# Kernel optimization log

Measured on AMD Instinct MI355X. Metric: run time of the kernel, lower is better.

Reference implementation:

```python
import jax, jax.numpy as jnp
import numpy as np

N_NODES = 50000
N_EDGES = 800000
D_FEAT = 64


def setup_inputs() -> dict:
    key = jax.random.key(0)
    k1, k2, k3, k4 = jax.random.split(key, 4)
    row_idx = jnp.sort(jax.random.randint(k1, (N_EDGES,), 0, N_NODES, dtype=jnp.int32))
    col_idx = jax.random.randint(k2, (N_EDGES,), 0, N_NODES, dtype=jnp.int32)
    vals = jax.random.uniform(k3, (N_EDGES,), dtype=jnp.float32)
    embeds = jax.random.normal(k4, (N_NODES, D_FEAT), dtype=jnp.float32)
    return {"row_idx": row_idx, "col_idx": col_idx, "vals": vals, "embeds": embeds}


def reference(row_idx, col_idx, vals, embeds):
    # SpMM: out[r] = sum_{e: row[e]==r} vals[e] * embeds[col[e]]
    gathered = vals[:, None] * embeds[col_idx]          # [E, D]
    out = jax.ops.segment_sum(gathered, row_idx, num_segments=N_NODES)  # [N, D]
    return out
```

## Files before the change

### kernel.cpp

```cpp
#include <hip/hip_runtime.h>


constexpr int N_NODES = 50000;
constexpr int N_EDGES = 800000;
constexpr int D_FEAT  = 64;

__global__ __launch_bounds__(256) void build_row_ptr_kernel(
    const int* __restrict__ row_idx,
    int*       __restrict__ row_ptr)
{
    const int e = blockIdx.x * blockDim.x + threadIdx.x;
    if (e >= N_EDGES) return;
    const int r     = row_idx[e];
    const int rprev = (e == 0) ? -1 : row_idx[e - 1];
    for (int q = rprev + 1; q <= r; ++q) row_ptr[q] = e;
    if (e == N_EDGES - 1) {
        for (int q = r + 1; q <= N_NODES; ++q) row_ptr[q] = N_EDGES;
    }
}

__global__ __launch_bounds__(256) void gcn_spmm_rows_kernel(
    const int*   __restrict__ row_ptr,
    const int*   __restrict__ col_idx,
    const float* __restrict__ vals,
    const float* __restrict__ embeds,
    float*       __restrict__ out)
{
    const int gtid = blockIdx.x * blockDim.x + threadIdx.x;
    const int row  = gtid >> 6;
    if (row >= N_NODES) return;
    const int lane = threadIdx.x & 63;
    const int q    = lane >> 4;
    const int f    = lane & 15;

    const int s = row_ptr[row];
    const int e = row_ptr[row + 1];

    const float4* __restrict__ emb4 = (const float4*)embeds;

    float4 a0 = make_float4(0.f, 0.f, 0.f, 0.f);
    float4 a1 = make_float4(0.f, 0.f, 0.f, 0.f);

    int base = s + q;
    for (; base + 4 < e; base += 8) {
        const int   c0 = col_idx[base];
        const float v0 = vals[base];
        const int   c1 = col_idx[base + 4];
        const float v1 = vals[base + 4];
        const float4 g0 = emb4[c0 * 16 + f];
        const float4 g1 = emb4[c1 * 16 + f];
        a0.x += v0 * g0.x; a0.y += v0 * g0.y; a0.z += v0 * g0.z; a0.w += v0 * g0.w;
        a1.x += v1 * g1.x; a1.y += v1 * g1.y; a1.z += v1 * g1.z; a1.w += v1 * g1.w;
    }
    if (base < e) {
        const int   c0 = col_idx[base];
        const float v0 = vals[base];
        const float4 g0 = emb4[c0 * 16 + f];
        a0.x += v0 * g0.x; a0.y += v0 * g0.y; a0.z += v0 * g0.z; a0.w += v0 * g0.w;
    }

    float x = a0.x + a1.x;
    float y = a0.y + a1.y;
    float z = a0.z + a1.z;
    float w = a0.w + a1.w;

    x += __shfl_xor(x, 16); x += __shfl_xor(x, 32);
    y += __shfl_xor(y, 16); y += __shfl_xor(y, 32);
    z += __shfl_xor(z, 16); z += __shfl_xor(z, 32);
    w += __shfl_xor(w, 16); w += __shfl_xor(w, 32);

    if (q == 0) {
        ((float4*)out)[row * 16 + f] = make_float4(x, y, z, w);
    }
}

extern "C" void kernel_launch(void* const* d_in, const int* in_sizes, int n_in,
                              void* d_out, int out_size, void* d_ws, size_t ws_size,
                              hipStream_t stream) {
    const int*   row_idx = (const int*)  d_in[0];
    const int*   col_idx = (const int*)  d_in[1];
    const float* vals    = (const float*)d_in[2];
    const float* embeds  = (const float*)d_in[3];
    float*       out     = (float*)      d_out;
    int*         row_ptr = (int*)        d_ws;

    {
        const int block  = 256;
        const int blocks = (N_EDGES + block - 1) / block;
        build_row_ptr_kernel<<<blocks, block, 0, stream>>>(row_idx, row_ptr);
    }
    {
        const int block  = 256;
        const int blocks = (N_NODES * 64 + block - 1) / block;
        gcn_spmm_rows_kernel<<<blocks, block, 0, stream>>>(row_ptr, col_idx, vals,
                                                           embeds, out);
    }
}
```

Baseline: 101.3 us.

## Split feature dimension into slices across blocks, one edge per lane group

Each wavefront now handles one row and only a 16-float slice of the features. Its 16 lane groups each take a different edge, and 4 lanes per group load a float4 each. Eight consecutive blocks cover two row-quads across four slices. This is meant to raise memory-level parallelism on rows averaging 16 edges, but each col_idx/vals element is now read four times, the grid is four times larger, and the final reduction needs more shuffle steps.

After: 129.0 us. 1.27x slower.

```diff
diff --git a/kernel.cpp b/kernel.cpp
--- a/kernel.cpp
+++ b/kernel.cpp
@@ -19,58 +19,54 @@
     }
 }
 
-__global__ __launch_bounds__(256) void gcn_spmm_rows_kernel(
+__global__ __launch_bounds__(256) void gcn_spmm_sliced_kernel(
     const int*   __restrict__ row_ptr,
     const int*   __restrict__ col_idx,
     const float* __restrict__ vals,
     const float* __restrict__ embeds,
     float*       __restrict__ out)
 {
-    const int gtid = blockIdx.x * blockDim.x + threadIdx.x;
-    const int row  = gtid >> 6;
+    const int b = blockIdx.x;
+    const int x = b & 7;
+    const int s = x & 3;
+    const int i = ((b >> 3) << 1) + (x >> 2);
+    const int row = (i << 2) + (threadIdx.x >> 6);
     if (row >= N_NODES) return;
+
     const int lane = threadIdx.x & 63;
-    const int q    = lane >> 4;
-    const int f    = lane & 15;
+    const int g    = lane >> 2;
+    const int h    = lane & 3;
 
-    const int s = row_ptr[row];
-    const int e = row_ptr[row + 1];
+    const int s_ = row_ptr[row];
+    const int e_ = row_ptr[row + 1];
 
     const float4* __restrict__ emb4 = (const float4*)embeds;
 
-    float4 a0 = make_float4(0.f, 0.f, 0.f, 0.f);
-    float4 a1 = make_float4(0.f, 0.f, 0.f, 0.f);
+    float4 acc = make_float4(0.f, 0.f, 0.f, 0.f);
 
-    int base = s + q;
-    for (; base + 4 < e; base += 8) {
-        const int   c0 = col_idx[base];
-        const float v0 = vals[base];
-        const int   c1 = col_idx[base + 4];
-        const float v1 = vals[base + 4];
-        const float4 g0 = emb4[c0 * 16 + f];
-        const float4 g1 = emb4[c1 * 16 + f];
-        a0.x += v0 * g0.x; a0.y += v0 * g0.y; a0.z += v0 * g0.z; a0.w += v0 * g0.w;
-        a1.x += v1 * g1.x; a1.y += v1 * g1.y; a1.z += v1 * g1.z; a1.w += v1 * g1.w;
-    }
-    if (base < e) {
-        const int   c0 = col_idx[base];
-        const float v0 = vals[base];
-        const float4 g0 = emb4[c0 * 16 + f];
-        a0.x += v0 * g0.x; a0.y += v0 * g0.y; a0.z += v0 * g0.z; a0.w += v0 * g0.w;
+    for (int base = s_; base < e_; base += 16) {
+        const int   edge = base + g;
+        const int   ce   = (edge < e_) ? edge : (e_ - 1);
+        const int   c    = col_idx[ce];
+        const float v    = (edge < e_) ? vals[ce] : 0.f;
+        const float4 gv  = emb4[c * 16 + s * 4 + h];
+        acc.x += v * gv.x;
+        acc.y += v * gv.y;
+        acc.z += v * gv.z;
+        acc.w += v * gv.w;
     }
 
-    float x = a0.x + a1.x;
-    float y = a0.y + a1.y;
-    float z = a0.z + a1.z;
-    float w = a0.w + a1.w;
+    acc.x += __shfl_xor(acc.x, 4);  acc.y += __shfl_xor(acc.y, 4);
+    acc.z += __shfl_xor(acc.z, 4);  acc.w += __shfl_xor(acc.w, 4);
+    acc.x += __shfl_xor(acc.x, 8);  acc.y += __shfl_xor(acc.y, 8);
+    acc.z += __shfl_xor(acc.z, 8);  acc.w += __shfl_xor(acc.w, 8);
+    acc.x += __shfl_xor(acc.x, 16); acc.y += __shfl_xor(acc.y, 16);
+    acc.z += __shfl_xor(acc.z, 16); acc.w += __shfl_xor(acc.w, 16);
+    acc.x += __shfl_xor(acc.x, 32); acc.y += __shfl_xor(acc.y, 32);
+    acc.z += __shfl_xor(acc.z, 32); acc.w += __shfl_xor(acc.w, 32);
 
-    x += __shfl_xor(x, 16); x += __shfl_xor(x, 32);
-    y += __shfl_xor(y, 16); y += __shfl_xor(y, 32);
-    z += __shfl_xor(z, 16); z += __shfl_xor(z, 32);
-    w += __shfl_xor(w, 16); w += __shfl_xor(w, 32);
-
-    if (q == 0) {
-        ((float4*)out)[row * 16 + f] = make_float4(x, y, z, w);
+    if (g == 0) {
+        ((float4*)out)[row * 16 + s * 4 + h] = acc;
     }
 }
 
@@ -91,8 +87,8 @@
     }
     {
         const int block  = 256;
-        const int blocks = (N_NODES * 64 + block - 1) / block;
-        gcn_spmm_rows_kernel<<<blocks, block, 0, stream>>>(row_ptr, col_idx, vals,
-                                                           embeds, out);
+        const int blocks = 50000;
+        gcn_spmm_sliced_kernel<<<blocks, block, 0, stream>>>(row_ptr, col_idx, vals,
+                                                             embeds, out);
     }
 }
```
